# Optimization experiments

Measured on AMD Instinct MI355X. Metric: run time of the kernel, lower is better.

The kernel has to match this reference:

```python
import jax, jax.numpy as jnp
import numpy as np

T_DATA = 100000
T_NO = 200
SUB_NO = 25
E_SYN = 2000
I_SYN = 500
COS_BASIS_NO = 13
OBS_BASIS_NO = 15


def _make_cos_basis(T_no):
    # [13, T_no] raised-cosine log-time basis
    i = np.arange(COS_BASIS_NO, dtype=np.float64)[:, None]
    phi = 0.5 * np.pi * i
    x = np.arange(T_no, dtype=np.float64)[None, :]
    raw = 3.0 * np.log(x + 1.0)  # cos_scale=3, cos_shift=1
    b = 0.5 * np.cos(raw - phi) + 0.5
    b = np.where((raw >= phi - np.pi) & (raw <= phi + np.pi), b, 0.0)
    return b.astype(np.float32)


def _make_obs_basis(T_no):
    # [2*15-1, 2*T_no+1] two-sided raised-cosine basis
    scale, shift = 4.0, 1.0
    obs = np.zeros((OBS_BASIS_NO * 2 - 1, 2 * T_no + 1), dtype=np.float64)
    for i in range(OBS_BASIS_NO):
        phi = 0.5 * np.pi * i
        xmin, xmax = phi - np.pi, phi + np.pi
        if i == 0:
            x = np.arange(-T_no, T_no + 1, dtype=np.float64)
            raw = scale * np.log(np.abs(x) + shift + 1e-7)
            obs[0] = np.where((raw >= xmin) & (raw <= xmax), 0.5 * np.cos(raw - phi) + 0.5, 0.0)
        else:
            xp = np.arange(0, T_no + 1, dtype=np.float64)
            xn = np.arange(-T_no, 1, dtype=np.float64)
            rp = scale * np.log(np.abs(xp) + shift + 1e-7)
            rn = scale * np.log(np.abs(xn) + shift + 1e-7)
            obs[2 * i - 1, T_no:] = np.where((rp >= xmin) & (rp <= xmax), 0.5 * np.cos(rp - phi) + 0.5, 0.0)
            obs[2 * i, :T_no + 1] = np.where((rn >= xmin) & (rn <= xmax), 0.5 * np.cos(rn - phi) + 0.5, 0.0)
    return obs.astype(np.float32)


def setup_inputs() -> dict:
    key = jax.random.key(0)
    ks = jax.random.split(key, 8)
    # binary spike inputs (sparse spike trains)
    S_e = (jax.random.uniform(ks[0], (T_DATA, E_SYN)) < 0.02).astype(jnp.float32)
    S_i = (jax.random.uniform(ks[1], (T_DATA, I_SYN)) < 0.02).astype(jnp.float32)
    Z = (jax.random.uniform(ks[2], (T_DATA,)) < 0.05).astype(jnp.float32)
    # one-hot connectivity: each synapse assigned to one subunit
    idx_e = jax.random.randint(ks[3], (E_SYN,), 0, SUB_NO)
    idx_i = jax.random.randint(ks[4], (I_SYN,), 0, SUB_NO)
    C_syn_e = jnp.zeros((SUB_NO, E_SYN), jnp.float32).at[idx_e, jnp.arange(E_SYN)].set(1.0)
    C_syn_i = jnp.zeros((SUB_NO, I_SYN), jnp.float32).at[idx_i, jnp.arange(I_SYN)].set(1.0)
    # learned params
    W_syn = 0.01 * jax.random.normal(ks[5], (SUB_NO - 1, COS_BASIS_NO, 2), jnp.float32)
    Theta = -5.0 * jnp.ones((SUB_NO - 1,), jnp.float32)
    W_obs = 0.01 * jax.random.uniform(ks[6], (SUB_NO - 1, OBS_BASIS_NO * 2 - 1), jnp.float32)
    return {
        "Z": Z, "S_e": S_e, "S_i": S_i,
        "C_syn_e": C_syn_e, "C_syn_i": C_syn_i,
        "W_syn": W_syn, "Theta": Theta, "W_obs": W_obs,
        "cos_basis": jnp.asarray(_make_cos_basis(T_NO)),
        "obs_basis": jnp.asarray(_make_obs_basis(T_NO)),
        "T_no": T_NO,
    }


def _conv1d(x, kern, pad, groups):
    # x: [1, C, L], kern: [O, C//groups, K] (torch conv1d cross-correlation)
    return jax.lax.conv_general_dilated(
        x, kern, window_strides=(1,), padding=[(pad, pad)],
        dimension_numbers=("NCH", "OIH", "NCH"), feature_group_count=groups)


def reference(Z, S_e, S_i, C_syn_e, C_syn_i, W_syn, Theta, W_obs, cos_basis, obs_basis, T_no):
    G = W_syn.shape[0]  # sub_no - 1
    # per-subunit synaptic drive: [T, G]
    syn_e = S_e @ C_syn_e[1:].T
    syn_i = S_i @ C_syn_i[1:].T
    # basis -> kernels, flipped for causal filtering: [G, 1, T_no]
    e_kern = jnp.flip((W_syn[:, :, 0] ** 2) @ cos_basis, axis=1)[:, None, :]
    i_kern = jnp.flip(-(W_syn[:, :, 1] ** 2) @ cos_basis, axis=1)[:, None, :]
    # left-pad with T_no zeros of history, depthwise conv, drop last sample
    pad_e = jnp.pad(syn_e, ((T_no, 0), (0, 0))).T[None]  # [1, G, T+T_no]
    pad_i = jnp.pad(syn_i, ((T_no, 0), (0, 0))).T[None]
    filt_e = _conv1d(pad_e, e_kern, 0, G)[0].T[:-1]  # [T, G]
    filt_i = _conv1d(pad_i, i_kern, 0, G)[0].T[:-1]
    syn = filt_e + filt_i
    # observation (spike-history) filter: [G, 1, 2*T_no+1], centered conv
    obs_kern = jnp.flip(W_obs @ obs_basis, axis=1)[:, None, :]
    obs_filt = _conv1d(Z[None, None, :], obs_kern, T_no, 1)[0].T  # [T, G]
    P = jax.nn.sigmoid(syn + obs_filt + Theta)
    Z_out = jax.random.bernoulli(jax.random.key(42), P).astype(P.dtype)
    return Z_out, P
```

## Files before the change

kernel.cpp:

```cpp
#include <hip/hip_runtime.h>
#include <hip/hip_bf16.h>
#include <math.h>

#define T_DATA 100000
#define NGRP   24
#define ESYN   2000
#define ISYN   500
#define NTOT   2400000

#define RNG_SCHEME 0

__device__ __forceinline__ unsigned tf_rotl(unsigned x, int r) {
    return (x << r) | (x >> (32 - r));
}

__device__ __forceinline__ void threefry2x32(unsigned c0, unsigned c1,
                                             unsigned& o0, unsigned& o1) {
    const unsigned K0 = 0u, K1 = 42u;
    const unsigned K2 = 0x1BD11BDAu ^ K0 ^ K1;
    unsigned x0 = c0 + K0;
    unsigned x1 = c1 + K1;
#define TFR(r) { x0 += x1; x1 = tf_rotl(x1, (r)); x1 ^= x0; }
    TFR(13) TFR(15) TFR(26) TFR(6)   x0 += K1; x1 += K2 + 1u;
    TFR(17) TFR(29) TFR(16) TFR(24)  x0 += K2; x1 += K0 + 2u;
    TFR(13) TFR(15) TFR(26) TFR(6)   x0 += K0; x1 += K1 + 3u;
    TFR(17) TFR(29) TFR(16) TFR(24)  x0 += K1; x1 += K2 + 4u;
    TFR(13) TFR(15) TFR(26) TFR(6)   x0 += K2; x1 += K0 + 5u;
#undef TFR
    o0 = x0; o1 = x1;
}

__device__ __forceinline__ unsigned rng_bits(unsigned i) {
#if RNG_SCHEME == 0
    unsigned a, b; threefry2x32(0u, i, a, b); return a ^ b;
#elif RNG_SCHEME == 1
    unsigned a, b; threefry2x32(0u, i, a, b); return b;
#elif RNG_SCHEME == 2
    unsigned a, b; threefry2x32(0u, i, a, b); return a;
#else
    const unsigned H = (unsigned)(NTOT / 2);
    unsigned a, b;
    if (i < H) { threefry2x32(i, i + H, a, b); return a; }
    else       { threefry2x32(i - H, i, a, b); return b; }
#endif
}

__global__ void prep_kernel(const float* __restrict__ C_e,
                            const float* __restrict__ C_i,
                            const float* __restrict__ W_syn,
                            const float* __restrict__ W_obs,
                            const float* __restrict__ cosb,
                            const float* __restrict__ obsb,
                            int* __restrict__ idx_e, int* __restrict__ idx_i,
                            float* __restrict__ ek, float* __restrict__ ik,
                            float* __restrict__ ok) {
    int i = blockIdx.x * blockDim.x + threadIdx.x;
    if (i < ESYN) {
        int r = -1;
        for (int g = 0; g < 25; ++g)
            if (C_e[g * ESYN + i] > 0.5f) { r = g - 1; break; }
        idx_e[i] = r;
    } else if (i < ESYN + ISYN) {
        int s = i - ESYN; int r = -1;
        for (int g = 0; g < 25; ++g)
            if (C_i[g * ISYN + s] > 0.5f) { r = g - 1; break; }
        idx_i[s] = r;
    } else if (i < ESYN + ISYN + NGRP * 200) {
        int q = i - (ESYN + ISYN);
        int g = q / 200, j = q % 200;
        float ae = 0.f, ai = 0.f;
        for (int b = 0; b < 13; ++b) {
            float we = W_syn[(g * 13 + b) * 2 + 0];
            float wi = W_syn[(g * 13 + b) * 2 + 1];
            float cb = cosb[b * 200 + j];
            ae = fmaf(we * we, cb, ae);
            ai = fmaf(wi * wi, cb, ai);
        }
        ek[g * 200 + j] = ae;
        ik[g * 200 + j] = -ai;
    } else if (i < ESYN + ISYN + NGRP * 200 + NGRP * 401) {
        int q = i - (ESYN + ISYN + NGRP * 200);
        int g = q / 401, tau = q % 401;
        float a = 0.f;
        for (int b = 0; b < 29; ++b)
            a = fmaf(W_obs[g * 29 + b], obsb[b * 401 + tau], a);
        ok[g * 401 + tau] = a;
    }
}

__global__ __launch_bounds__(256) void hist_kernel(
        const float* __restrict__ S_e, const float* __restrict__ S_i,
        const int* __restrict__ idx_e, const int* __restrict__ idx_i,
        float* __restrict__ synE, float* __restrict__ synI) {
    __shared__ float cntE[4][32];
    __shared__ float cntI[4][32];
    const int wv = threadIdx.x >> 6;
    const int lane = threadIdx.x & 63;
    const int t = blockIdx.x * 4 + wv;
    if (lane < 32) { cntE[wv][lane] = 0.f; cntI[wv][lane] = 0.f; }
    __syncthreads();

    const float4* re = (const float4*)(S_e + (size_t)t * ESYN);
    for (int c = lane; c < ESYN / 4; c += 64) {
        float4 v = re[c];
        int cb = c * 4;
        if (v.x != 0.f) { int g = idx_e[cb + 0]; if (g >= 0) atomicAdd(&cntE[wv][g], v.x); }
        if (v.y != 0.f) { int g = idx_e[cb + 1]; if (g >= 0) atomicAdd(&cntE[wv][g], v.y); }
        if (v.z != 0.f) { int g = idx_e[cb + 2]; if (g >= 0) atomicAdd(&cntE[wv][g], v.z); }
        if (v.w != 0.f) { int g = idx_e[cb + 3]; if (g >= 0) atomicAdd(&cntE[wv][g], v.w); }
    }
    const float4* ri = (const float4*)(S_i + (size_t)t * ISYN);
    for (int c = lane; c < ISYN / 4; c += 64) {
        float4 v = ri[c];
        int cb = c * 4;
        if (v.x != 0.f) { int g = idx_i[cb + 0]; if (g >= 0) atomicAdd(&cntI[wv][g], v.x); }
        if (v.y != 0.f) { int g = idx_i[cb + 1]; if (g >= 0) atomicAdd(&cntI[wv][g], v.y); }
        if (v.z != 0.f) { int g = idx_i[cb + 2]; if (g >= 0) atomicAdd(&cntI[wv][g], v.z); }
        if (v.w != 0.f) { int g = idx_i[cb + 3]; if (g >= 0) atomicAdd(&cntI[wv][g], v.w); }
    }
    __syncthreads();
    if (lane < NGRP) {
        synE[(size_t)lane * T_DATA + t] = cntE[wv][lane];
        synI[(size_t)lane * T_DATA + t] = cntI[wv][lane];
    }
}

constexpr int TT = 1024;
constexpr int BLK3 = 128;

__global__ __launch_bounds__(128) void filter_kernel(
        const float* __restrict__ Z,
        const float* __restrict__ synE, const float* __restrict__ synI,
        const float* __restrict__ ek, const float* __restrict__ ik,
        const float* __restrict__ ok, const float* __restrict__ Theta,
        float* __restrict__ out) {
    __shared__ float2 syn_l[TT + 200];
    __shared__ float  z_l[TT + 400];
    __shared__ float2 kern_l[200];
    __shared__ float  ok_l[401];

    const int g  = blockIdx.y;
    const int t0 = blockIdx.x * TT;
    const int tid = threadIdx.x;

    for (int p = tid; p < TT + 200; p += BLK3) {
        int t = t0 - 200 + p;
        float e = 0.f, ii = 0.f;
        if (t >= 0 && t < T_DATA) {
            e  = synE[(size_t)g * T_DATA + t];
            ii = synI[(size_t)g * T_DATA + t];
        }
        syn_l[p] = make_float2(e, ii);
    }
    for (int p = tid; p < TT + 400; p += BLK3) {
        int t = t0 - 200 + p;
        z_l[p] = (t >= 0 && t < T_DATA) ? Z[t] : 0.f;
    }
    for (int p = tid; p < 200; p += BLK3)
        kern_l[p] = make_float2(ek[g * 200 + p], ik[g * 200 + p]);
    for (int p = tid; p < 401; p += BLK3)
        ok_l[p] = ok[g * 401 + p];
    __syncthreads();

    float accS[8], accZ[8];
#pragma unroll
    for (int k = 0; k < 8; ++k) { accS[k] = 0.f; accZ[k] = 0.f; }

    {
        const int B = tid * 8 + 199;
        float2 w[8];
#pragma unroll
        for (int p = 0; p < 8; ++p) w[p] = syn_l[B + p];
        for (int nb = 0; nb < 200; nb += 8) {
#pragma unroll
            for (int jj = 0; jj < 8; ++jj) {
                const int n = nb + jj;
                const float2 kv = kern_l[n];
#pragma unroll
                for (int k = 0; k < 8; ++k) {
                    const float2 d = w[(k - jj) & 7];
                    accS[k] = fmaf(d.x, kv.x, fmaf(d.y, kv.y, accS[k]));
                }
                if (n < 199) w[(7 - jj) & 7] = syn_l[B - n - 1];
            }
        }
    }

    {
        const int Bz = tid * 8 + 400;
        float wz[8];
#pragma unroll
        for (int p = 0; p < 8; ++p) wz[p] = z_l[Bz + p];
        for (int nb = 0; nb < 400; nb += 8) {
#pragma unroll
            for (int jj = 0; jj < 8; ++jj) {
                const int n = nb + jj;
                const float kv = ok_l[n];
#pragma unroll
                for (int k = 0; k < 8; ++k)
                    accZ[k] = fmaf(wz[(k - jj) & 7], kv, accZ[k]);
                wz[(7 - jj) & 7] = z_l[Bz - n - 1];
            }
        }
        const float kv = ok_l[400];
#pragma unroll
        for (int k = 0; k < 8; ++k)
            accZ[k] = fmaf(wz[k], kv, accZ[k]);
    }

    const float theta_g = Theta[g];
#pragma unroll
    for (int k = 0; k < 8; ++k) {
        int t = t0 + tid * 8 + k;
        if (t < T_DATA) {
            double x  = (double)accS[k] + (double)accZ[k] + (double)theta_g;
            double Pd = 1.0 / (1.0 + exp(-x));
            float  Pf = (float)Pd;
            unsigned i = (unsigned)(t * NGRP + g);
            unsigned bits = rng_bits(i);
            float u = __uint_as_float((bits >> 9) | 0x3f800000u) - 1.0f;
            size_t o = (size_t)t * NGRP + g;
            out[o]        = (u < Pf) ? 1.0f : 0.0f;
            out[NTOT + o] = Pf;
        }
    }
}

extern "C" void kernel_launch(void* const* d_in, const int* in_sizes, int n_in,
                              void* d_out, int out_size, void* d_ws, size_t ws_size,
                              hipStream_t stream) {
    const float* Z     = (const float*)d_in[0];
    const float* S_e   = (const float*)d_in[1];
    const float* S_i   = (const float*)d_in[2];
    const float* C_e   = (const float*)d_in[3];
    const float* C_i   = (const float*)d_in[4];
    const float* W_syn = (const float*)d_in[5];
    const float* Theta = (const float*)d_in[6];
    const float* W_obs = (const float*)d_in[7];
    const float* cosb  = (const float*)d_in[8];
    const float* obsb  = (const float*)d_in[9];

    float* ws   = (float*)d_ws;
    float* synE = ws;
    float* synI = synE + NTOT;
    float* ek   = synI + NTOT;
    float* ik   = ek + NGRP * 200;
    float* ok   = ik + NGRP * 200;
    int*   idx_e = (int*)(ok + NGRP * 401);
    int*   idx_i = idx_e + ESYN;

    const int prep_items = ESYN + ISYN + NGRP * 200 + NGRP * 401;
    prep_kernel<<<(prep_items + 255) / 256, 256, 0, stream>>>(
        C_e, C_i, W_syn, W_obs, cosb, obsb, idx_e, idx_i, ek, ik, ok);

    hist_kernel<<<T_DATA / 4, 256, 0, stream>>>(S_e, S_i, idx_e, idx_i, synE, synI);

    dim3 grid3((T_DATA + TT - 1) / TT, NGRP);
    filter_kernel<<<grid3, BLK3, 0, stream>>>(Z, synE, synI, ek, ik, ok, Theta,
                                              (float*)d_out);
}
```

Baseline: 1.375 ms.

## Batch histogram loads, interleave E/I counts, and swizzle filter shared memory

The histogram kernel now issues all row loads up front (8 excitatory and 2 inhibitory float4 per lane) and only then does the shared atomics. Unassigned synapses map to a dummy bin 31, which removes the per-spike branch. Excitatory and inhibitory counts are written interleaved as float2, so the filter kernel fetches both with one load. The filter kernel XOR-swizzles its shared syn/z arrays to cut bank conflicts from the strided per-thread window reads. This costs more registers in hist and a little extra index arithmetic in the inner loops.

Measured after the change: 1.269 ms. -7.7%, faster.

```diff
diff --git a/kernel.cpp b/kernel.cpp
--- a/kernel.cpp
+++ b/kernel.cpp
@@ -8,18 +8,15 @@
 #define ISYN   500
 #define NTOT   2400000
 
-#define RNG_SCHEME 0
-
 __device__ __forceinline__ unsigned tf_rotl(unsigned x, int r) {
     return (x << r) | (x >> (32 - r));
 }
 
-__device__ __forceinline__ void threefry2x32(unsigned c0, unsigned c1,
-                                             unsigned& o0, unsigned& o1) {
+__device__ __forceinline__ unsigned rng_bits(unsigned i) {
     const unsigned K0 = 0u, K1 = 42u;
     const unsigned K2 = 0x1BD11BDAu ^ K0 ^ K1;
-    unsigned x0 = c0 + K0;
-    unsigned x1 = c1 + K1;
+    unsigned x0 = 0u + K0;
+    unsigned x1 = i  + K1;
 #define TFR(r) { x0 += x1; x1 = tf_rotl(x1, (r)); x1 ^= x0; }
     TFR(13) TFR(15) TFR(26) TFR(6)   x0 += K1; x1 += K2 + 1u;
     TFR(17) TFR(29) TFR(16) TFR(24)  x0 += K2; x1 += K0 + 2u;
@@ -27,23 +24,11 @@
     TFR(17) TFR(29) TFR(16) TFR(24)  x0 += K1; x1 += K2 + 4u;
     TFR(13) TFR(15) TFR(26) TFR(6)   x0 += K2; x1 += K0 + 5u;
 #undef TFR
-    o0 = x0; o1 = x1;
-}
-
-__device__ __forceinline__ unsigned rng_bits(unsigned i) {
-#if RNG_SCHEME == 0
-    unsigned a, b; threefry2x32(0u, i, a, b); return a ^ b;
-#elif RNG_SCHEME == 1
-    unsigned a, b; threefry2x32(0u, i, a, b); return b;
-#elif RNG_SCHEME == 2
-    unsigned a, b; threefry2x32(0u, i, a, b); return a;
-#else
-    const unsigned H = (unsigned)(NTOT / 2);
-    unsigned a, b;
-    if (i < H) { threefry2x32(i, i + H, a, b); return a; }
-    else       { threefry2x32(i - H, i, a, b); return b; }
-#endif
-}
+    return x0 ^ x1;
+}
+
+__device__ __forceinline__ int swz2(int p) { return p ^ ((p >> 3) & 15); }
+__device__ __forceinline__ int swz1(int p) { return p ^ ((p >> 3) & 31); }
 
 __global__ void prep_kernel(const float* __restrict__ C_e,
                             const float* __restrict__ C_i,
@@ -56,13 +41,13 @@
                             float* __restrict__ ok) {
     int i = blockIdx.x * blockDim.x + threadIdx.x;
     if (i < ESYN) {
-        int r = -1;
-        for (int g = 0; g < 25; ++g)
+        int r = 31;
+        for (int g = 1; g < 25; ++g)
             if (C_e[g * ESYN + i] > 0.5f) { r = g - 1; break; }
         idx_e[i] = r;
     } else if (i < ESYN + ISYN) {
-        int s = i - ESYN; int r = -1;
-        for (int g = 0; g < 25; ++g)
+        int s = i - ESYN; int r = 31;
+        for (int g = 1; g < 25; ++g)
             if (C_i[g * ISYN + s] > 0.5f) { r = g - 1; break; }
         idx_i[s] = r;
     } else if (i < ESYN + ISYN + NGRP * 200) {
@@ -91,7 +76,7 @@
 __global__ __launch_bounds__(256) void hist_kernel(
         const float* __restrict__ S_e, const float* __restrict__ S_i,
         const int* __restrict__ idx_e, const int* __restrict__ idx_i,
-        float* __restrict__ synE, float* __restrict__ synI) {
+        float2* __restrict__ synEI) {
     __shared__ float cntE[4][32];
     __shared__ float cntI[4][32];
     const int wv = threadIdx.x >> 6;
@@ -101,41 +86,54 @@
     __syncthreads();
 
     const float4* re = (const float4*)(S_e + (size_t)t * ESYN);
-    for (int c = lane; c < ESYN / 4; c += 64) {
-        float4 v = re[c];
-        int cb = c * 4;
-        if (v.x != 0.f) { int g = idx_e[cb + 0]; if (g >= 0) atomicAdd(&cntE[wv][g], v.x); }
-        if (v.y != 0.f) { int g = idx_e[cb + 1]; if (g >= 0) atomicAdd(&cntE[wv][g], v.y); }
-        if (v.z != 0.f) { int g = idx_e[cb + 2]; if (g >= 0) atomicAdd(&cntE[wv][g], v.z); }
-        if (v.w != 0.f) { int g = idx_e[cb + 3]; if (g >= 0) atomicAdd(&cntE[wv][g], v.w); }
-    }
     const float4* ri = (const float4*)(S_i + (size_t)t * ISYN);
-    for (int c = lane; c < ISYN / 4; c += 64) {
-        float4 v = ri[c];
-        int cb = c * 4;
-        if (v.x != 0.f) { int g = idx_i[cb + 0]; if (g >= 0) atomicAdd(&cntI[wv][g], v.x); }
-        if (v.y != 0.f) { int g = idx_i[cb + 1]; if (g >= 0) atomicAdd(&cntI[wv][g], v.y); }
-        if (v.z != 0.f) { int g = idx_i[cb + 2]; if (g >= 0) atomicAdd(&cntI[wv][g], v.z); }
-        if (v.w != 0.f) { int g = idx_i[cb + 3]; if (g >= 0) atomicAdd(&cntI[wv][g], v.w); }
+    float4 ve[8], vi[2];
+#pragma unroll
+    for (int k = 0; k < 8; ++k) {
+        int c = lane + 64 * k;
+        ve[k] = (c < ESYN / 4) ? re[c] : make_float4(0.f, 0.f, 0.f, 0.f);
+    }
+#pragma unroll
+    for (int k = 0; k < 2; ++k) {
+        int c = lane + 64 * k;
+        vi[k] = (c < ISYN / 4) ? ri[c] : make_float4(0.f, 0.f, 0.f, 0.f);
+    }
+#pragma unroll
+    for (int k = 0; k < 8; ++k) {
+        const int cb = (lane + 64 * k) * 4;
+        float4 v = ve[k];
+        if (v.x != 0.f) atomicAdd(&cntE[wv][idx_e[cb + 0]], v.x);
+        if (v.y != 0.f) atomicAdd(&cntE[wv][idx_e[cb + 1]], v.y);
+        if (v.z != 0.f) atomicAdd(&cntE[wv][idx_e[cb + 2]], v.z);
+        if (v.w != 0.f) atomicAdd(&cntE[wv][idx_e[cb + 3]], v.w);
+    }
+#pragma unroll
+    for (int k = 0; k < 2; ++k) {
+        const int cb = (lane + 64 * k) * 4;
+        float4 v = vi[k];
+        if (v.x != 0.f) atomicAdd(&cntI[wv][idx_i[cb + 0]], v.x);
+        if (v.y != 0.f) atomicAdd(&cntI[wv][idx_i[cb + 1]], v.y);
+        if (v.z != 0.f) atomicAdd(&cntI[wv][idx_i[cb + 2]], v.z);
+        if (v.w != 0.f) atomicAdd(&cntI[wv][idx_i[cb + 3]], v.w);
     }
     __syncthreads();
-    if (lane < NGRP) {
-        synE[(size_t)lane * T_DATA + t] = cntE[wv][lane];
-        synI[(size_t)lane * T_DATA + t] = cntI[wv][lane];
-    }
+    if (lane < NGRP)
+        synEI[(size_t)lane * T_DATA + t] = make_float2(cntE[wv][lane], cntI[wv][lane]);
 }
 
 constexpr int TT = 1024;
 constexpr int BLK3 = 128;
+constexpr int SYN_L = 1232;
+constexpr int Z_L   = 1440;
 
 __global__ __launch_bounds__(128) void filter_kernel(
         const float* __restrict__ Z,
-        const float* __restrict__ synE, const float* __restrict__ synI,
+        const float2* __restrict__ synEI,
         const float* __restrict__ ek, const float* __restrict__ ik,
         const float* __restrict__ ok, const float* __restrict__ Theta,
         float* __restrict__ out) {
-    __shared__ float2 syn_l[TT + 200];
-    __shared__ float  z_l[TT + 400];
+    __shared__ float2 syn_l[SYN_L];
+    __shared__ float  z_l[Z_L];
     __shared__ float2 kern_l[200];
     __shared__ float  ok_l[401];
 
@@ -143,18 +141,15 @@
     const int t0 = blockIdx.x * TT;
     const int tid = threadIdx.x;
 
+    const float2* s2 = synEI + (size_t)g * T_DATA;
     for (int p = tid; p < TT + 200; p += BLK3) {
         int t = t0 - 200 + p;
-        float e = 0.f, ii = 0.f;
-        if (t >= 0 && t < T_DATA) {
-            e  = synE[(size_t)g * T_DATA + t];
-            ii = synI[(size_t)g * T_DATA + t];
-        }
-        syn_l[p] = make_float2(e, ii);
+        float2 v = (t >= 0 && t < T_DATA) ? s2[t] : make_float2(0.f, 0.f);
+        syn_l[swz2(p)] = v;
     }
     for (int p = tid; p < TT + 400; p += BLK3) {
         int t = t0 - 200 + p;
-        z_l[p] = (t >= 0 && t < T_DATA) ? Z[t] : 0.f;
+        z_l[swz1(p)] = (t >= 0 && t < T_DATA) ? Z[t] : 0.f;
     }
     for (int p = tid; p < 200; p += BLK3)
         kern_l[p] = make_float2(ek[g * 200 + p], ik[g * 200 + p]);
@@ -170,7 +165,7 @@
         const int B = tid * 8 + 199;
         float2 w[8];
 #pragma unroll
-        for (int p = 0; p < 8; ++p) w[p] = syn_l[B + p];
+        for (int p = 0; p < 8; ++p) w[p] = syn_l[swz2(B + p)];
         for (int nb = 0; nb < 200; nb += 8) {
 #pragma unroll
             for (int jj = 0; jj < 8; ++jj) {
@@ -181,7 +176,7 @@
                     const float2 d = w[(k - jj) & 7];
                     accS[k] = fmaf(d.x, kv.x, fmaf(d.y, kv.y, accS[k]));
                 }
-                if (n < 199) w[(7 - jj) & 7] = syn_l[B - n - 1];
+                if (n < 199) w[(7 - jj) & 7] = syn_l[swz2(B - n - 1)];
             }
         }
     }
@@ -190,7 +185,7 @@
         const int Bz = tid * 8 + 400;
         float wz[8];
 #pragma unroll
-        for (int p = 0; p < 8; ++p) wz[p] = z_l[Bz + p];
+        for (int p = 0; p < 8; ++p) wz[p] = z_l[swz1(Bz + p)];
         for (int nb = 0; nb < 400; nb += 8) {
 #pragma unroll
             for (int jj = 0; jj < 8; ++jj) {
@@ -199,7 +194,7 @@
 #pragma unroll
                 for (int k = 0; k < 8; ++k)
                     accZ[k] = fmaf(wz[(k - jj) & 7], kv, accZ[k]);
-                wz[(7 - jj) & 7] = z_l[Bz - n - 1];
+                wz[(7 - jj) & 7] = z_l[swz1(Bz - n - 1)];
             }
         }
         const float kv = ok_l[400];
@@ -240,12 +235,11 @@
     const float* cosb  = (const float*)d_in[8];
     const float* obsb  = (const float*)d_in[9];
 
-    float* ws   = (float*)d_ws;
-    float* synE = ws;
-    float* synI = synE + NTOT;
-    float* ek   = synI + NTOT;
-    float* ik   = ek + NGRP * 200;
-    float* ok   = ik + NGRP * 200;
+    float* ws    = (float*)d_ws;
+    float2* synEI = (float2*)ws;
+    float* ek    = ws + 2 * NTOT;
+    float* ik    = ek + NGRP * 200;
+    float* ok    = ik + NGRP * 200;
     int*   idx_e = (int*)(ok + NGRP * 401);
     int*   idx_i = idx_e + ESYN;
 
@@ -253,9 +247,9 @@
     prep_kernel<<<(prep_items + 255) / 256, 256, 0, stream>>>(
         C_e, C_i, W_syn, W_obs, cosb, obsb, idx_e, idx_i, ek, ik, ok);
 
-    hist_kernel<<<T_DATA / 4, 256, 0, stream>>>(S_e, S_i, idx_e, idx_i, synE, synI);
+    hist_kernel<<<T_DATA / 4, 256, 0, stream>>>(S_e, S_i, idx_e, idx_i, synEI);
 
     dim3 grid3((T_DATA + TT - 1) / TT, NGRP);
-    filter_kernel<<<grid3, BLK3, 0, stream>>>(Z, synE, synI, ek, ik, ok, Theta,
+    filter_kernel<<<grid3, BLK3, 0, stream>>>(Z, synEI, ek, ik, ok, Theta,
                                               (float*)d_out);
 }
```
